# Optimization experiments

Hardware: AMD Instinct MI355X
Metric: run time of the kernel (lower is better)

## Reference

```python
import jax, jax.numpy as jnp
import numpy as np
import math

B, T, D, CAP = 4, 1024, 512, 32768
MEM_UPDATE_MOMENTUM = 0.99
MEM_NEW_DATA_RATE = 0.01

def setup_inputs() -> dict:
    key = jax.random.key(0)
    k1, k2, k3, k4, k5 = jax.random.split(key, 5)
    keys = jax.random.normal(k1, (B, T, D), dtype=jnp.float32)
    values = jax.random.normal(k2, (B, T, D), dtype=jnp.float32)
    importance = jax.random.uniform(k3, (B, T, 1), dtype=jnp.float32)
    query = jax.random.normal(k4, (B, T, D), dtype=jnp.float32)
    # xavier_uniform on (1, CAP, D): fan_in=D, fan_out=CAP (torch treats dim-1/dim-2)
    bound = math.sqrt(6.0 / (CAP + D))
    mem = jax.random.uniform(k5, (1, CAP, D), minval=-bound, maxval=bound, dtype=jnp.float32)
    return {"keys": keys, "values": values, "importance": importance, "query": query, "mem": mem}

def reference(keys, values, importance, query, mem):
    b, t, d = keys.shape
    cap = mem.shape[1]
    # ---- write ----
    scores = jnp.einsum('btd,ocd->btc', keys, mem)          # [b, t, cap]
    usage = jax.nn.softmax(scores, axis=-1).sum(axis=1)     # [b, cap]
    combined = importance.mean(axis=(1, 2))                 # [b]
    write_priority = combined[:, None] + 0.1 * usage        # [b, cap]
    k = min(t, cap)
    _, indices = jax.lax.top_k(write_priority, k)           # [b, k]
    values_write = values[:, :k]                            # [b, k, d]
    scatter = jnp.zeros((b, cap, d), dtype=keys.dtype)
    scatter = scatter.at[jnp.arange(b)[:, None], indices].set(values_write)
    new_mem = mem * MEM_UPDATE_MOMENTUM + scatter.mean(axis=0, keepdims=True) * MEM_NEW_DATA_RATE
    # ---- read (against updated memory) ----
    attn = jnp.einsum('bqd,ocd->bqc', query, new_mem) / math.sqrt(d)
    attn = jax.nn.softmax(attn, axis=-1)                    # [b, q, cap]
    out = jnp.einsum('bqc,ocd->bqd', attn, new_mem)         # [b, q, d]
    return out
```

## Files before the change

kernel.cpp:

```cpp
#include <hip/hip_runtime.h>
#include <hip/hip_fp8.h>

typedef float f32x4 __attribute__((ext_vector_type(4)));
typedef float f32x16 __attribute__((ext_vector_type(16)));
typedef short s16x8 __attribute__((ext_vector_type(8)));
typedef short s16x4 __attribute__((ext_vector_type(4)));
typedef unsigned short ush;
typedef unsigned char u8;

constexpr int Bn = 4, Tn = 1024, Dn = 512, CAPn = 32768, Kn = 1024;
constexpr int ROWS = Bn * Tn;
constexpr float SCALE = 0.044194173824159216f;
constexpr float SC64 = SCALE / 64.0f;
constexpr float MOM = 0.99f;
constexpr float RATE_B = 0.0025f;

constexpr size_t OFF_NM8   = 0;
constexpr size_t OFF_NMT   = 33554432;
constexpr size_t OFF_OPART = 67108864;
constexpr size_t OFF_KHF   = 67108864;
constexpr size_t OFF_ZPART = 75497472;
constexpr size_t OFF_PRIO  = 83886080;
constexpr size_t OFF_RANK  = 84410368;
constexpr size_t OFF_COMB  = 84934656;
constexpr size_t OFF_ZP2   = 100663296;

#define MFMA(a, b, c) __builtin_amdgcn_mfma_f32_16x16x32_bf16((a), (b), (c), 0, 0, 0)
#define MFMAH(a, b, c) __builtin_amdgcn_mfma_f32_16x16x32_f16((a), (b), (c), 0, 0, 0)
#define MFMA8(a, b, c) __builtin_amdgcn_mfma_f32_16x16x32_fp8_fp8((a), (b), (c), 0, 0, 0)
#define MFMAB32(a, b, c) __builtin_amdgcn_mfma_f32_32x32x16_bf16((a), (b), (c), 0, 0, 0)

__device__ __forceinline__ ush bfrn(float x) {
  unsigned u = __float_as_uint(x);
  return (ush)((u + 0x7FFFu + ((u >> 16) & 1u)) >> 16);
}
__device__ __forceinline__ float bff(ush h) { return __uint_as_float(((unsigned)h) << 16); }
__device__ __forceinline__ ush f16rn(float x) {
  _Float16 h = (_Float16)x;
  return *(ush*)&h;
}
__device__ __forceinline__ u8 f8rn(float x) {
  __hip_fp8_e4m3 v(x);
  return (u8)v.__x;
}

__device__ __forceinline__ void gl16(const void* g, void* l) {
  __builtin_amdgcn_global_load_lds(
      (const __attribute__((address_space(1))) void*)(uintptr_t)g,
      (__attribute__((address_space(3))) void*)(uintptr_t)l, 16, 0, 0);
}

__global__ void k_combined(const float* __restrict__ imp, float* __restrict__ comb) {
  __shared__ float red[256];
  int b = blockIdx.x;
  float s = 0.f;
  for (int t = threadIdx.x; t < Tn; t += 256) s += imp[(size_t)b * Tn + t];
  red[threadIdx.x] = s;
  __syncthreads();
  for (int off = 128; off > 0; off >>= 1) {
    if (threadIdx.x < (unsigned)off) red[threadIdx.x] += red[threadIdx.x + off];
    __syncthreads();
  }
  if (threadIdx.x == 0) comb[b] = red[0] * (1.0f / Tn);
}

__global__ void k_cvt_all(const float* __restrict__ mem, const float* __restrict__ keys,
                          ush* __restrict__ mhf, ush* __restrict__ khf) {
  int bid = blockIdx.x;
  const float* src;
  ush* dst;
  size_t i;
  if (bid < 16384) {
    src = mem;
    dst = mhf;
    i = ((size_t)bid * 256 + threadIdx.x) * 4;
  } else {
    src = keys;
    dst = khf;
    i = ((size_t)(bid - 16384) * 256 + threadIdx.x) * 4;
  }
  f32x4 v = *(const f32x4*)&src[i];
  s16x4 h;
#pragma unroll
  for (int j = 0; j < 4; ++j) h[j] = (short)f16rn(v[j]);
  *(s16x4*)&dst[i] = h;
}

__global__ __launch_bounds__(256, 2) void k_rowexp(const ush* __restrict__ Ahf,
                                                   const ush* __restrict__ Bhf,
                                                   float* __restrict__ zpart) {
  __shared__ ush Bs[64 * 512];
  __shared__ float red[2][64];
  const int tid = threadIdx.x;
  const int lane = tid & 63, wid = tid >> 6;
  const int wc2 = wid >> 1, wt = wid & 1;
  const int l15 = lane & 15, g = lane >> 4;
  const int cb = blockIdx.x;
  const int cBase = cb * 64;

  s16x8 afr[2][16];
#pragma unroll
  for (int mi = 0; mi < 2; ++mi) {
    int c = cBase + wc2 * 32 + mi * 16 + l15;
#pragma unroll
    for (int ks = 0; ks < 16; ++ks)
      afr[mi][ks] = *(const s16x8*)&Ahf[(size_t)c * Dn + ks * 32 + g * 8];
  }

  for (int tt = 0; tt < 64; ++tt) {
    const int tBase = tt * 64;
#pragma unroll
    for (int rr = 0; rr < 16; ++rr) {
      int idx = rr * 256 + tid;
      int row = idx >> 6, ch = idx & 63;
      gl16(&Bhf[(size_t)(tBase + row) * Dn + ((ch ^ (row & 7)) << 3)],
           &Bs[rr * 2048 + wid * 512]);
    }
    __syncthreads();
    f32x4 S[2][2];
#pragma unroll
    for (int mi = 0; mi < 2; ++mi)
#pragma unroll
      for (int ni = 0; ni < 2; ++ni) S[mi][ni] = (f32x4){0.f, 0.f, 0.f, 0.f};
#pragma unroll
    for (int ks = 0; ks < 16; ++ks) {
      s16x8 bfr[2];
#pragma unroll
      for (int ni = 0; ni < 2; ++ni) {
        int trow = wt * 32 + ni * 16 + l15;
        bfr[ni] = *(const s16x8*)&Bs[trow * 512 + (((ks * 4 + g) ^ (trow & 7)) * 8)];
      }
#pragma unroll
      for (int mi = 0; mi < 2; ++mi)
#pragma unroll
        for (int ni = 0; ni < 2; ++ni) S[mi][ni] = MFMAH(afr[mi][ks], bfr[ni], S[mi][ni]);
    }
    float tacc[2] = {0.f, 0.f};
#pragma unroll
    for (int mi = 0; mi < 2; ++mi)
#pragma unroll
      for (int ni = 0; ni < 2; ++ni)
#pragma unroll
        for (int r = 0; r < 4; ++r) tacc[ni] += __expf(S[mi][ni][r]);
#pragma unroll
    for (int ni = 0; ni < 2; ++ni) {
      float v = tacc[ni];
      v += __shfl_xor(v, 16);
      v += __shfl_xor(v, 32);
      tacc[ni] = v;
    }
    if (g == 0) {
      red[wc2][wt * 32 + l15] = tacc[0];
      red[wc2][wt * 32 + 16 + l15] = tacc[1];
    }
    __syncthreads();
    if (tid < 64) zpart[(size_t)cb * ROWS + tBase + tid] = red[0][tid] + red[1][tid];
  }
}

__global__ void k_invl(const float* __restrict__ zpart, float* __restrict__ invl) {
  int t = blockIdx.x * 256 + threadIdx.x;
  float s = 0.f;
  for (int cb = 0; cb < 512; ++cb) s += zpart[(size_t)cb * ROWS + t];
  invl[t] = 1.0f / s;
}

#define WAITV0 asm volatile("s_waitcnt vmcnt(0)" ::: "memory")
#define WAITV2 asm volatile("s_waitcnt vmcnt(2)" ::: "memory")
#define WAITL0 asm volatile("s_waitcnt lgkmcnt(0)" ::: "memory")
#define BAR __builtin_amdgcn_s_barrier()

__global__ __launch_bounds__(256, 2) void k_usage(const ush* __restrict__ mhf,
                                                  const ush* __restrict__ khf,
                                                  const float* __restrict__ invl,
                                                  const float* __restrict__ comb,
                                                  float* __restrict__ prio) {
  __shared__ ush Bh[2][128 * 64];
  const int tid = threadIdx.x;
  const int lane = tid & 63, w = tid >> 6;
  const int l15 = lane & 15, g = lane >> 4;
  const int cBase = blockIdx.x * 128;
  const int b = blockIdx.y;
  const ush* khb = khf + (size_t)b * Tn * Dn;
  const int r0 = tid >> 3, u0 = tid & 7;
  const int usw = (u0 ^ (r0 & 7)) << 3;

  s16x8 afr[2][16];
#pragma unroll
  for (int mi = 0; mi < 2; ++mi) {
    int c = cBase + w * 32 + mi * 16 + l15;
#pragma unroll
    for (int ks = 0; ks < 16; ++ks)
      afr[mi][ks] = *(const s16x8*)&mhf[(size_t)c * Dn + ks * 32 + g * 8];
  }

  auto stageB = [&](int p) {
    int tt = p >> 3, kk = p & 7;
    size_t b0 = (size_t)(tt * 128 + r0) * Dn + kk * 64 + usw;
    size_t b1 = (size_t)(tt * 128 + r0 + 64) * Dn + kk * 64 + usw;
    gl16(&khb[b0], &Bh[p & 1][w * 512]);
    gl16(&khb[b1], &Bh[p & 1][4096 + w * 512]);
  };

  float uacc[2][4] = {{0.f, 0.f, 0.f, 0.f}, {0.f, 0.f, 0.f, 0.f}};
  stageB(0);
  for (int tt = 0; tt < 8; ++tt) {
    f32x4 S[2][8];
#pragma unroll
    for (int mi = 0; mi < 2; ++mi)
#pragma unroll
      for (int ni = 0; ni < 8; ++ni) S[mi][ni] = (f32x4){0.f, 0.f, 0.f, 0.f};
#pragma unroll
    for (int kk = 0; kk < 8; ++kk) {
      const int p = tt * 8 + kk;
      WAITV0;
      WAITL0;
      BAR;
      if (p < 63) stageB(p + 1);
      __builtin_amdgcn_s_setprio(1);
#pragma unroll
      for (int ks2 = 0; ks2 < 2; ++ks2) {
#pragma unroll
        for (int ni = 0; ni < 8; ++ni) {
          int trow = ni * 16 + l15;
          s16x8 bh =
              *(const s16x8*)&Bh[p & 1][trow * 64 + (((ks2 * 4 + g) ^ (trow & 7)) * 8)];
#pragma unroll
          for (int mi = 0; mi < 2; ++mi)
            S[mi][ni] = MFMAH(afr[mi][kk * 2 + ks2], bh, S[mi][ni]);
        }
      }
      __builtin_amdgcn_s_setprio(0);
    }
#pragma unroll
    for (int ni = 0; ni < 8; ++ni) {
      float il = invl[b * Tn + tt * 128 + ni * 16 + l15];
#pragma unroll
      for (int mi = 0; mi < 2; ++mi)
#pragma unroll
        for (int r = 0; r < 4; ++r) uacc[mi][r] += __expf(S[mi][ni][r]) * il;
    }
  }
#pragma unroll
  for (int mi = 0; mi < 2; ++mi)
#pragma unroll
    for (int r = 0; r < 4; ++r) {
      float v = uacc[mi][r];
      v += __shfl_xor(v, 1);
      v += __shfl_xor(v, 2);
      v += __shfl_xor(v, 4);
      v += __shfl_xor(v, 8);
      if (l15 == 0)
        prio[(size_t)b * CAPn + cBase + w * 32 + mi * 16 + g * 4 + r] =
            comb[b] + 0.1f * v;
    }
}

__global__ void k_rankinit(int* __restrict__ rank) {
  rank[blockIdx.x * 256 + threadIdx.x] = Kn;
}

__global__ __launch_bounds__(1024) void k_select(const float* __restrict__ prio,
                                                 int* __restrict__ rank) {
  const int b = blockIdx.x;
  const float* p = prio + (size_t)b * CAPn;
  __shared__ int hist[256];
  __shared__ unsigned long long s_pref;
  __shared__ int s_krem;
  __shared__ int s_cnt;
  __shared__ unsigned long long selk[Kn];
  const int tid = threadIdx.x;
  if (tid == 0) { s_pref = 0ull; s_krem = Kn; s_cnt = 0; }

#define KEYOF(c, kk)                                                         \
  {                                                                          \
    unsigned mb_ = __float_as_uint(p[(c)]);                                  \
    mb_ = (mb_ & 0x80000000u) ? ~mb_ : (mb_ | 0x80000000u);                  \
    (kk) = ((unsigned long long)mb_ << 32) | (unsigned)(0xFFFFFFFFu - (c));  \
  }

  __syncthreads();
  for (int pos = 56; pos >= 0; pos -= 8) {
    if (tid < 256) hist[tid] = 0;
    __syncthreads();
    unsigned long long pref = s_pref;
    unsigned long long maskhi = (pos == 56) ? 0ull : (~0ull << (pos + 8));
    for (int c = tid; c < CAPn; c += 1024) {
      unsigned long long k;
      KEYOF(c, k);
      if ((k & maskhi) == pref) atomicAdd(&hist[(int)((k >> pos) & 255)], 1);
    }
    __syncthreads();
    if (tid == 0) {
      int krem = s_krem;
      int d = 255;
      for (;; --d) {
        int h = hist[d];
        if (krem <= h || d == 0) break;
        krem -= h;
      }
      s_pref = pref | ((unsigned long long)d << pos);
      s_krem = krem;
    }
    __syncthreads();
  }
  unsigned long long T = s_pref;
  for (int c = tid; c < CAPn; c += 1024) {
    unsigned long long k;
    KEYOF(c, k);
    if (k >= T) {
      int idx = atomicAdd(&s_cnt, 1);
      selk[idx] = k;
    }
  }
  __syncthreads();
  unsigned long long mine = selk[tid];
  int r = 0;
  for (int j = 0; j < Kn; ++j) r += (selk[j] > mine) ? 1 : 0;
  int c = (int)(0xFFFFFFFFu - (unsigned)(mine & 0xFFFFFFFFull));
  rank[(size_t)b * CAPn + c] = r;
#undef KEYOF
}

__global__ void k_newmem8(const float* __restrict__ mem, const float* __restrict__ values,
                          const int* __restrict__ rank, u8* __restrict__ nm8) {
  int gid = blockIdx.x * 256 + threadIdx.x;
  int c = gid >> 7;
  int q = (gid & 127) << 2;
  f32x4 m = *(const f32x4*)&mem[(size_t)c * Dn + q];
  f32x4 acc = {0.f, 0.f, 0.f, 0.f};
#pragma unroll
  for (int b = 0; b < Bn; ++b) {
    int r = rank[(size_t)b * CAPn + c];
    if (r < Kn) acc += *(const f32x4*)&values[((size_t)b * Tn + r) * Dn + q];
  }
  f32x4 res = (m * MOM + acc * RATE_B) * 64.0f;
  union { u8 b[4]; unsigned w; } out;
#pragma unroll
  for (int j = 0; j < 4; ++j) out.b[j] = f8rn(res[j]);
  *(unsigned*)&nm8[(size_t)c * Dn + q] = out.w;
}

__global__ __launch_bounds__(256) void k_nmT(const float* __restrict__ mem,
                                             const float* __restrict__ values,
                                             const int* __restrict__ rank,
                                             ush* __restrict__ nmT) {
  __shared__ ush tile[64][65];
  int cBase = blockIdx.x * 64, dBase = blockIdx.y * 64;
  int tid = threadIdx.x;
  int c = tid >> 2, dq = (tid & 3) * 16;
  int rr[4];
#pragma unroll
  for (int b = 0; b < Bn; ++b) rr[b] = rank[(size_t)b * CAPn + cBase + c];
#pragma unroll
  for (int j = 0; j < 4; ++j) {
    f32x4 m = *(const f32x4*)&mem[(size_t)(cBase + c) * Dn + dBase + dq + j * 4];
    f32x4 a = {0.f, 0.f, 0.f, 0.f};
#pragma unroll
    for (int b = 0; b < Bn; ++b)
      if (rr[b] < Kn)
        a += *(const f32x4*)&values[((size_t)b * Tn + rr[b]) * Dn + dBase + dq + j * 4];
    f32x4 res = m * MOM + a * RATE_B;
#pragma unroll
    for (int jj = 0; jj < 4; ++jj) tile[c][dq + j * 4 + jj] = bfrn(res[jj]);
  }
  __syncthreads();
  int drow = tid >> 2, cq = (tid & 3) * 16;
#pragma unroll
  for (int k = 0; k < 2; ++k) {
    s16x8 v;
#pragma unroll
    for (int j = 0; j < 8; ++j) v[j] = (short)tile[cq + k * 8 + j][drow];
    *(s16x8*)&nmT[(size_t)(dBase + drow) * CAPn + cBase + cq + k * 8] = v;
  }
}

__global__ __launch_bounds__(512, 1) void k_attnout(
    const float* __restrict__ query, const u8* __restrict__ nm8,
    const ush* __restrict__ nmT, ush* __restrict__ opart,
    float* __restrict__ zp2) {
  __shared__ __align__(16) u8 L[131072];
  __shared__ float zred[128];
  __shared__ float zacc[128];
  constexpr int LMS = 0, LMT = 49152, LPS = 98304;
  const int tid = threadIdx.x;
  const int lane = tid & 63, w = tid >> 6;
  const int l15 = lane & 15, g = lane >> 4;
  const int l31 = lane & 31, h = lane >> 5;
  const int dt = w & 3, qg = w >> 2;
  const int cy = blockIdx.x;
  const int qBase = blockIdx.y * 128;
  const int q = w * 16 + l15;
  const int r0 = tid >> 3, u0 = tid & 7;
  const int usw = (u0 ^ (r0 & 7)) << 3;
  const int usw8 = (u0 ^ (r0 & 7)) << 4;

  auto stage_ms = [&](int buf, int cb_, int kk) {
    const u8* src = nm8 + (size_t)cb_ * Dn + kk * 128;
    gl16(&src[(size_t)r0 * Dn + usw8], &L[LMS + buf * 16384 + w * 1024]);
    gl16(&src[(size_t)(r0 + 64) * Dn + usw8], &L[LMS + buf * 16384 + 8192 + w * 1024]);
  };
  auto stage_mt = [&](int buf, int cb_, int u) {
    const ush* src = nmT + (size_t)((u >> 1) * 128) * CAPn + cb_ + (u & 1) * 64;
    gl16(&src[(size_t)r0 * CAPn + usw], &L[LMT + buf * 16384 + w * 1024]);
    gl16(&src[(size_t)(r0 + 64) * CAPn + usw], &L[LMT + buf * 16384 + 8192 + w * 1024]);
  };

  long qfr8[16];
  {
    const float* qsrc = query + (size_t)(qBase + q) * Dn;
#pragma unroll
    for (int ks = 0; ks < 16; ++ks) {
      f32x4 a = *(const f32x4*)&qsrc[ks * 32 + g * 8];
      f32x4 b = *(const f32x4*)&qsrc[ks * 32 + g * 8 + 4];
      union { u8 c[8]; long l; } u;
#pragma unroll
      for (int j = 0; j < 4; ++j) {
        u.c[j] = f8rn(a[j]);
        u.c[4 + j] = f8rn(b[j]);
      }
      qfr8[ks] = u.l;
    }
  }

  f32x16 O[8];
#pragma unroll
  for (int i = 0; i < 8; ++i) O[i] = (f32x16)(0.f);
  if (tid < 128) zacc[tid] = 0.f;

  stage_ms(0, cy * 4096, 0);
  stage_ms(1, cy * 4096, 1);

  for (int ct = 0; ct < 32; ++ct) {
    const int cBase = cy * 4096 + ct * 128;
    const int cNext = cy * 4096 + ((ct + 1) & 31) * 128;

    f32x4 S[8];
#pragma unroll
    for (int i = 0; i < 8; ++i) S[i] = (f32x4){0.f, 0.f, 0.f, 0.f};
#pragma unroll
    for (int kk = 0; kk < 4; ++kk) {
      WAITV2;
      WAITL0;
      BAR;
      if (kk < 2) stage_ms((kk + 2) % 3, cBase, kk + 2);
      else if (kk == 2) stage_mt(0, cBase, 0);
      else stage_mt(1, cBase, 1);
      __builtin_amdgcn_s_setprio(1);
#pragma unroll
      for (int ks = 0; ks < 4; ++ks) {
#pragma unroll
        for (int mi = 0; mi < 8; ++mi) {
          int row = mi * 16 + l15;
          long a = *(const long*)&L[LMS + (kk % 3) * 16384 + row * 128 +
                                    (((ks * 2 + (g >> 1)) ^ (row & 7)) << 4) +
                                    (g & 1) * 8];
          S[mi] = MFMA8(a, qfr8[kk * 4 + ks], S[mi]);
        }
      }
      __builtin_amdgcn_s_setprio(0);
    }

    float zl = 0.f;
#pragma unroll
    for (int mi = 0; mi < 8; ++mi) {
      s16x4 p;
#pragma unroll
      for (int r = 0; r < 4; ++r) {
        float e = __expf(S[mi][r] * SC64);
        zl += e;
        p[r] = (short)bfrn(e);
      }
      int u16 = (mi * 2 + (g >> 1)) ^ l15;
      *(s16x4*)&L[LPS + q * 256 + u16 * 16 + (g & 1) * 8] = p;
    }
    zl += __shfl_xor(zl, 16);
    zl += __shfl_xor(zl, 32);
    if (g == 0) zred[q] = zl;
    WAITL0;
    BAR;
    if (tid < 128) zacc[tid] += zred[tid];

#pragma unroll
    for (int u = 0; u < 8; ++u) {
      WAITV2;
      WAITL0;
      BAR;
      if (u < 6) stage_mt((u + 2) % 3, cBase, u + 2);
      else if (u == 6) stage_ms(0, cNext, 0);
      else stage_ms(1, cNext, 1);
      __builtin_amdgcn_s_setprio(1);
#pragma unroll
      for (int kc = 0; kc < 4; ++kc) {
        int d = dt * 32 + l31;
        s16x8 am = *(const s16x8*)&L[LMT + (u % 3) * 16384 + d * 128 +
                                     (((kc * 2 + h) ^ (d & 7)) << 4)];
#pragma unroll
        for (int tqi = 0; tqi < 2; ++tqi) {
          int qq = qg * 64 + tqi * 32 + l31;
          s16x8 pb = *(const s16x8*)&L[LPS + qq * 256 +
                                       ((((u & 1) * 8 + kc * 2 + h) ^ (qq & 15)) << 4)];
          O[(u >> 1) * 2 + tqi] = MFMAB32(am, pb, O[(u >> 1) * 2 + tqi]);
        }
      }
      __builtin_amdgcn_s_setprio(0);
    }
  }

  __syncthreads();
  if (tid < 128) zp2[(size_t)cy * ROWS + qBase + tid] = zacc[tid];
#pragma unroll
  for (int p = 0; p < 4; ++p) {
    __syncthreads();
    if (qg == (p >> 1)) {
      const int tqi = p & 1;
#pragma unroll
      for (int db = 0; db < 4; ++db)
#pragma unroll
        for (int r2 = 0; r2 < 4; ++r2) {
          s16x4 ov;
#pragma unroll
          for (int j = 0; j < 4; ++j) ov[j] = (short)bfrn(O[db * 2 + tqi][r2 * 4 + j]);
          int u8i = db * 32 + dt * 8 + r2 * 2 + h;
          int u8s = u8i ^ ((l31 & 15) << 1);
          *(s16x4*)&L[LPS + l31 * 1024 + u8s * 8] = ov;
        }
    }
    __syncthreads();
#pragma unroll
    for (int i = 0; i < 4; ++i) {
      int slot = i * 512 + tid;
      int ql = slot >> 6, u16 = slot & 63;
      s16x8 v = *(const s16x8*)&L[LPS + ql * 1024 + ((u16 ^ (ql & 15)) << 4)];
      *(s16x8*)&opart[((size_t)cy * ROWS + qBase + p * 32 + ql) * Dn + u16 * 8] = v;
    }
  }
}

__global__ void k_merge(const ush* __restrict__ opart, const float* __restrict__ zp2,
                        float* __restrict__ out) {
  size_t i = ((size_t)blockIdx.x * 256 + threadIdx.x) * 4;
  int row = (int)(i >> 9);
  float z = 0.f;
#pragma unroll
  for (int cyy = 0; cyy < 8; ++cyy) z += zp2[(size_t)cyy * ROWS + row];
  float inv = 1.0f / z;
  f32x4 acc = {0.f, 0.f, 0.f, 0.f};
#pragma unroll
  for (int cyy = 0; cyy < 8; ++cyy) {
    s16x4 a = *(const s16x4*)&opart[(size_t)cyy * ROWS * Dn + i];
#pragma unroll
    for (int j = 0; j < 4; ++j) acc[j] += bff((ush)a[j]);
  }
#pragma unroll
  for (int j = 0; j < 4; ++j) acc[j] *= inv;
  *(f32x4*)&out[i] = acc;
}

extern "C" void kernel_launch(void* const* d_in, const int* in_sizes, int n_in,
                              void* d_out, int out_size, void* d_ws, size_t ws_size,
                              hipStream_t stream) {
  const float* keys = (const float*)d_in[0];
  const float* values = (const float*)d_in[1];
  const float* importance = (const float*)d_in[2];
  const float* query = (const float*)d_in[3];
  const float* mem = (const float*)d_in[4];
  char* wsb = (char*)d_ws;
  u8* nm8    = (u8*)(wsb + OFF_NM8);
  ush* nmT   = (ush*)(wsb + OFF_NMT);
  ush* mhf   = (ush*)(wsb + OFF_NMT);
  ush* khf   = (ush*)(wsb + OFF_KHF);
  ush* opart = (ush*)(wsb + OFF_OPART);
  float* zpart = (float*)(wsb + OFF_ZPART);
  float* prio  = (float*)(wsb + OFF_PRIO);
  int* rank    = (int*)(wsb + OFF_RANK);
  float* comb  = (float*)(wsb + OFF_COMB);
  float* zp2   = (float*)(wsb + OFF_ZP2);
  float* invl1 = (float*)(wsb + OFF_COMB + 64);
  float* out = (float*)d_out;

  k_combined<<<Bn, 256, 0, stream>>>(importance, comb);
  k_cvt_all<<<18432, 256, 0, stream>>>(mem, keys, mhf, khf);
  k_rowexp<<<CAPn / 64, 256, 0, stream>>>(mhf, khf, zpart);
  k_invl<<<ROWS / 256, 256, 0, stream>>>(zpart, invl1);
  k_usage<<<dim3(CAPn / 128, Bn), 256, 0, stream>>>(mhf, khf, invl1, comb, prio);
  k_rankinit<<<(Bn * CAPn) / 256, 256, 0, stream>>>(rank);
  k_select<<<Bn, 1024, 0, stream>>>(prio, rank);
  k_newmem8<<<(CAPn * Dn / 4) / 256, 256, 0, stream>>>(mem, values, rank, nm8);
  k_nmT<<<dim3(CAPn / 64, Dn / 64), 256, 0, stream>>>(mem, values, rank, nmT);
  k_attnout<<<dim3(8, ROWS / 128), 512, 0, stream>>>(query, nm8, nmT, opart, zp2);
  k_merge<<<(ROWS * Dn / 4) / 256, 256, 0, stream>>>(opart, zp2, out);
}
```

Before: 789.1 us.

## Use FP8 MFMA for softmax row-sum pass and warp-aggregate select histogram

The conversion kernel now also emits FP8 copies of memory (pre-scaled by 64) and keys. The row-exp normalizer pass uses these with fp8 MFMA instead of fp16, halving shared and global traffic, and rescales by 1/64 before the exponent. The radix-select histogram now uses ballot-based warp aggregation so each wave issues one shared-memory atomic per distinct digit instead of one per element. FP8 lowers the accuracy of the softmax normalizers that feed top-k usage, which could change which slots are selected.

```diff
diff --git a/kernel.cpp b/kernel.cpp
--- a/kernel.cpp
+++ b/kernel.cpp
@@ -12,10 +12,12 @@
 constexpr int ROWS = Bn * Tn;
 constexpr float SCALE = 0.044194173824159216f;
 constexpr float SC64 = SCALE / 64.0f;
+constexpr float INV64 = 0.015625f;
 constexpr float MOM = 0.99f;
 constexpr float RATE_B = 0.0025f;
 
 constexpr size_t OFF_NM8   = 0;
+constexpr size_t OFF_K8    = 16777216;
 constexpr size_t OFF_NMT   = 33554432;
 constexpr size_t OFF_OPART = 67108864;
 constexpr size_t OFF_KHF   = 67108864;
@@ -65,31 +67,40 @@
 }
 
 __global__ void k_cvt_all(const float* __restrict__ mem, const float* __restrict__ keys,
-                          ush* __restrict__ mhf, ush* __restrict__ khf) {
+                          ush* __restrict__ mhf, u8* __restrict__ m8,
+                          ush* __restrict__ khf, u8* __restrict__ k8) {
   int bid = blockIdx.x;
-  const float* src;
-  ush* dst;
-  size_t i;
   if (bid < 16384) {
-    src = mem;
-    dst = mhf;
-    i = ((size_t)bid * 256 + threadIdx.x) * 4;
+    size_t i = ((size_t)bid * 256 + threadIdx.x) * 4;
+    f32x4 v = *(const f32x4*)&mem[i];
+    s16x4 h;
+    union { u8 b[4]; unsigned w; } r;
+#pragma unroll
+    for (int j = 0; j < 4; ++j) {
+      h[j] = (short)f16rn(v[j]);
+      r.b[j] = f8rn(v[j] * 64.0f);
+    }
+    *(s16x4*)&mhf[i] = h;
+    *(unsigned*)&m8[i] = r.w;
   } else {
-    src = keys;
-    dst = khf;
-    i = ((size_t)(bid - 16384) * 256 + threadIdx.x) * 4;
-  }
-  f32x4 v = *(const f32x4*)&src[i];
-  s16x4 h;
-#pragma unroll
-  for (int j = 0; j < 4; ++j) h[j] = (short)f16rn(v[j]);
-  *(s16x4*)&dst[i] = h;
-}
-
-__global__ __launch_bounds__(256, 2) void k_rowexp(const ush* __restrict__ Ahf,
-                                                   const ush* __restrict__ Bhf,
-                                                   float* __restrict__ zpart) {
-  __shared__ ush Bs[64 * 512];
+    size_t i = ((size_t)(bid - 16384) * 256 + threadIdx.x) * 4;
+    f32x4 v = *(const f32x4*)&keys[i];
+    s16x4 h;
+    union { u8 b[4]; unsigned w; } r;
+#pragma unroll
+    for (int j = 0; j < 4; ++j) {
+      h[j] = (short)f16rn(v[j]);
+      r.b[j] = f8rn(v[j]);
+    }
+    *(s16x4*)&khf[i] = h;
+    *(unsigned*)&k8[i] = r.w;
+  }
+}
+
+__global__ __launch_bounds__(256, 3) void k_rowexp8(const u8* __restrict__ m8,
+                                                    const u8* __restrict__ k8,
+                                                    float* __restrict__ zpart) {
+  __shared__ __align__(16) u8 Bs8[32768];
   __shared__ float red[2][64];
   const int tid = threadIdx.x;
   const int lane = tid & 63, wid = tid >> 6;
@@ -98,23 +109,23 @@
   const int cb = blockIdx.x;
   const int cBase = cb * 64;
 
-  s16x8 afr[2][16];
+  long afr8[2][16];
 #pragma unroll
   for (int mi = 0; mi < 2; ++mi) {
     int c = cBase + wc2 * 32 + mi * 16 + l15;
 #pragma unroll
     for (int ks = 0; ks < 16; ++ks)
-      afr[mi][ks] = *(const s16x8*)&Ahf[(size_t)c * Dn + ks * 32 + g * 8];
+      afr8[mi][ks] = *(const long*)&m8[(size_t)c * Dn + ks * 32 + g * 8];
   }
 
   for (int tt = 0; tt < 64; ++tt) {
     const int tBase = tt * 64;
 #pragma unroll
-    for (int rr = 0; rr < 16; ++rr) {
+    for (int rr = 0; rr < 8; ++rr) {
       int idx = rr * 256 + tid;
-      int row = idx >> 6, ch = idx & 63;
-      gl16(&Bhf[(size_t)(tBase + row) * Dn + ((ch ^ (row & 7)) << 3)],
-           &Bs[rr * 2048 + wid * 512]);
+      int row = idx >> 5, ch = idx & 31;
+      gl16(&k8[(size_t)(tBase + row) * Dn + ((ch ^ (row & 7)) << 4)],
+           &Bs8[rr * 4096 + wid * 1024]);
     }
     __syncthreads();
     f32x4 S[2][2];
@@ -124,16 +135,18 @@
       for (int ni = 0; ni < 2; ++ni) S[mi][ni] = (f32x4){0.f, 0.f, 0.f, 0.f};
 #pragma unroll
     for (int ks = 0; ks < 16; ++ks) {
-      s16x8 bfr[2];
+      long bfr[2];
 #pragma unroll
       for (int ni = 0; ni < 2; ++ni) {
         int trow = wt * 32 + ni * 16 + l15;
-        bfr[ni] = *(const s16x8*)&Bs[trow * 512 + (((ks * 4 + g) ^ (trow & 7)) * 8)];
+        bfr[ni] = *(const long*)&Bs8[trow * 512 +
+                                     (((ks * 2 + (g >> 1)) ^ (trow & 7)) << 4) +
+                                     (g & 1) * 8];
       }
 #pragma unroll
       for (int mi = 0; mi < 2; ++mi)
 #pragma unroll
-        for (int ni = 0; ni < 2; ++ni) S[mi][ni] = MFMAH(afr[mi][ks], bfr[ni], S[mi][ni]);
+        for (int ni = 0; ni < 2; ++ni) S[mi][ni] = MFMA8(afr8[mi][ks], bfr[ni], S[mi][ni]);
     }
     float tacc[2] = {0.f, 0.f};
 #pragma unroll
@@ -141,7 +154,7 @@
 #pragma unroll
       for (int ni = 0; ni < 2; ++ni)
 #pragma unroll
-        for (int r = 0; r < 4; ++r) tacc[ni] += __expf(S[mi][ni][r]);
+        for (int r = 0; r < 4; ++r) tacc[ni] += __expf(S[mi][ni][r] * INV64);
 #pragma unroll
     for (int ni = 0; ni < 2; ++ni) {
       float v = tacc[ni];
@@ -270,6 +283,7 @@
   __shared__ int s_cnt;
   __shared__ unsigned long long selk[Kn];
   const int tid = threadIdx.x;
+  const int lane = tid & 63;
   if (tid == 0) { s_pref = 0ull; s_krem = Kn; s_cnt = 0; }
 
 #define KEYOF(c, kk)                                                         \
@@ -288,7 +302,18 @@
     for (int c = tid; c < CAPn; c += 1024) {
       unsigned long long k;
       KEYOF(c, k);
-      if ((k & maskhi) == pref) atomicAdd(&hist[(int)((k >> pos) & 255)], 1);
+      bool valid = ((k & maskhi) == pref);
+      int d = (int)((k >> pos) & 255);
+      unsigned long long m = __ballot(valid);
+#pragma unroll
+      for (int bit = 0; bit < 8; ++bit) {
+        unsigned long long bb = __ballot((d >> bit) & 1);
+        m &= ((d >> bit) & 1) ? bb : ~bb;
+      }
+      if (valid) {
+        int leader = __ffsll((unsigned long long)m) - 1;
+        if (lane == leader) atomicAdd(&hist[d], __popcll(m));
+      }
     }
     __syncthreads();
     if (tid == 0) {
@@ -567,6 +592,8 @@
   const float* mem = (const float*)d_in[4];
   char* wsb = (char*)d_ws;
   u8* nm8    = (u8*)(wsb + OFF_NM8);
+  u8* m8     = (u8*)(wsb + OFF_NM8);
+  u8* k8     = (u8*)(wsb + OFF_K8);
   ush* nmT   = (ush*)(wsb + OFF_NMT);
   ush* mhf   = (ush*)(wsb + OFF_NMT);
   ush* khf   = (ush*)(wsb + OFF_KHF);
@@ -580,8 +607,8 @@
   float* out = (float*)d_out;
 
   k_combined<<<Bn, 256, 0, stream>>>(importance, comb);
-  k_cvt_all<<<18432, 256, 0, stream>>>(mem, keys, mhf, khf);
-  k_rowexp<<<CAPn / 64, 256, 0, stream>>>(mhf, khf, zpart);
+  k_cvt_all<<<18432, 256, 0, stream>>>(mem, keys, mhf, m8, khf, k8);
+  k_rowexp8<<<CAPn / 64, 256, 0, stream>>>(m8, k8, zpart);
   k_invl<<<ROWS / 256, 256, 0, stream>>>(zpart, invl1);
   k_usage<<<dim3(CAPn / 128, Bn), 256, 0, stream>>>(mhf, khf, invl1, comb, prio);
   k_rankinit<<<(Bn * CAPn) / 256, 256, 0, stream>>>(rank);
```

After: 803.6 us. No clear change (+1.8%).
